# Performance work log

Measured on AMD Instinct MI355X. Metric: run time of the kernel, lower is better.

Reference implementation:

```python
import jax, jax.numpy as jnp
import numpy as np
import math

B, S, D, H = 2, 2048, 1024, 16
HD = D // H  # head_dim = 64


def setup_inputs() -> dict:
    rng = jax.random.key(0)
    ks = jax.random.split(rng, 11)
    std = 1.0 / math.sqrt(D)
    inp = {
        "query": jax.random.normal(ks[0], (B, S, D), dtype=jnp.float32),
        "key": jax.random.normal(ks[1], (B, S, D), dtype=jnp.float32),
        "value": jax.random.normal(ks[2], (B, S, D), dtype=jnp.float32),
        # causal mask: True = masked (ignored), matching masked_fill semantics
        "mask": jnp.triu(jnp.ones((S, S), dtype=bool), k=1),
        "wq": jax.random.normal(ks[3], (D, D), dtype=jnp.float32) * std,
        "bq": jnp.zeros((D,), dtype=jnp.float32),
        "wk": jax.random.normal(ks[4], (D, D), dtype=jnp.float32) * std,
        "bk": jnp.zeros((D,), dtype=jnp.float32),
        "wv": jax.random.normal(ks[5], (D, D), dtype=jnp.float32) * std,
        "bv": jnp.zeros((D,), dtype=jnp.float32),
        "wo": jax.random.normal(ks[6], (D, D), dtype=jnp.float32) * std,
        "bo": jnp.zeros((D,), dtype=jnp.float32),
    }
    return inp


def reference(query, key, value, mask, wq, bq, wk, bk, wv, bv, wo, bo):
    # Linear projections (torch Linear: x @ W.T + b)
    q = jnp.einsum('bsd,ed->bse', query, wq) + bq
    k = jnp.einsum('bsd,ed->bse', key, wk) + bk
    v = jnp.einsum('bsd,ed->bse', value, wv) + bv
    # split heads: (B, S, D) -> (B, H, S, HD)
    q = q.reshape(B, S, H, HD).transpose(0, 2, 1, 3)
    k = k.reshape(B, S, H, HD).transpose(0, 2, 1, 3)
    v = v.reshape(B, S, H, HD).transpose(0, 2, 1, 3)
    # naive attention: materialize full (B, H, Sq, Sk) scores
    scores = jnp.einsum('bhqd,bhkd->bhqk', q, k) / jnp.sqrt(jnp.float32(HD))
    scores = jnp.where(mask[None, None, :, :], -jnp.inf, scores)
    attn = jax.nn.softmax(scores, axis=-1)
    out = jnp.einsum('bhqk,bhkd->bhqd', attn, v)
    out = out.transpose(0, 2, 1, 3).reshape(B, S, D)
    return jnp.einsum('bsd,ed->bse', out, wo) + bo
```

## Files before the change

### kernel.cpp

```cpp
#include <hip/hip_runtime.h>
#include <stdint.h>

#define B_ 2
#define S_ 2048
#define D_ 1024
#define H_ 16
#define HD_ 64
#define M_TOT (B_*S_)

typedef __bf16 bf16;
typedef bf16 bf16x8 __attribute__((ext_vector_type(8)));
typedef float f32x4 __attribute__((ext_vector_type(4)));
typedef float f32x16 __attribute__((ext_vector_type(16)));
typedef unsigned int u32;
typedef unsigned int u32x4v __attribute__((ext_vector_type(4)));

__device__ __forceinline__ void gload_lds16(const void* g, void* l) {
    __builtin_amdgcn_global_load_lds((const __attribute__((address_space(1))) void*)g,
                                     (__attribute__((address_space(3))) void*)l, 16, 0, 0);
}

__device__ __forceinline__ u32 cvtpk_bf16(float lo, float hi) {
    u32 d;
    asm("v_cvt_pk_bf16_f32 %0, %1, %2" : "=v"(d) : "v"(lo), "v"(hi));
    return d;
}

__global__ __launch_bounds__(256) void cvt_kernel(
    const float* __restrict__ q, const float* __restrict__ k, const float* __restrict__ v,
    const float* __restrict__ wq, const float* __restrict__ wk,
    const float* __restrict__ wv, const float* __restrict__ wo,
    bf16* __restrict__ xq, bf16* __restrict__ xk, bf16* __restrict__ xv,
    bf16* __restrict__ wqb, bf16* __restrict__ wkb, bf16* __restrict__ wvb, bf16* __restrict__ wob)
{
    const float* src; bf16* dst; int n;
    switch (blockIdx.y) {
        case 0: src=q;  dst=xq;  n=M_TOT*D_; break;
        case 1: src=k;  dst=xk;  n=M_TOT*D_; break;
        case 2: src=v;  dst=xv;  n=M_TOT*D_; break;
        case 3: src=wq; dst=wqb; n=D_*D_;    break;
        case 4: src=wk; dst=wkb; n=D_*D_;    break;
        case 5: src=wv; dst=wvb; n=D_*D_;    break;
        default: src=wo; dst=wob; n=D_*D_;   break;
    }
    int i = (blockIdx.x*blockDim.x + threadIdx.x)*8;
    if (i >= n) return;
    const f32x4* s4 = (const f32x4*)(src + i);
    f32x4 a = s4[0], b = s4[1];
    bf16x8 o;
    #pragma unroll
    for (int j = 0; j < 4; ++j) { o[j] = (bf16)a[j]; o[j+4] = (bf16)b[j]; }
    *(bf16x8*)(dst + i) = o;
}

__device__ __forceinline__ void gemm_mainloop(const bf16* __restrict__ A, const bf16* __restrict__ Wt,
                                              int brow, int bcol, bf16* As, bf16* Bs,
                                              f32x4 (&acc)[4][4])
{
    const int tid = threadIdx.x;
    const int l = tid & 63, w = tid >> 6;
    const int wr = w >> 1, wc = w & 1;
    const int lr = l & 15, lq = l >> 4;

    for (int k0 = 0; k0 < D_; k0 += 32) {
        #pragma unroll
        for (int i = 0; i < 2; ++i) {
            int id = i*256 + tid;
            int row = id >> 2, c8 = (id & 3) << 3;
            gload_lds16(A  + (size_t)(brow + row)*D_ + k0 + c8, As + id*8);
            gload_lds16(Wt + (size_t)(bcol + row)*D_ + k0 + c8, Bs + id*8);
        }
        __syncthreads();
        bf16x8 af[4], bf[4];
        #pragma unroll
        for (int m = 0; m < 4; ++m)
            af[m] = *(const bf16x8*)&As[(wr*64 + m*16 + lr)*32 + lq*8];
        #pragma unroll
        for (int n = 0; n < 4; ++n)
            bf[n] = *(const bf16x8*)&Bs[(wc*64 + n*16 + lr)*32 + lq*8];
        #pragma unroll
        for (int m = 0; m < 4; ++m)
            #pragma unroll
            for (int n = 0; n < 4; ++n)
                acc[m][n] = __builtin_amdgcn_mfma_f32_16x16x32_bf16(af[m], bf[n], acc[m][n], 0, 0, 0);
        __syncthreads();
    }
}

__global__ __launch_bounds__(256) void gemm_qkv(
    const bf16* __restrict__ xq, const bf16* __restrict__ xk, const bf16* __restrict__ xv,
    const bf16* __restrict__ wqb, const bf16* __restrict__ wkb, const bf16* __restrict__ wvb,
    const float* __restrict__ bq, const float* __restrict__ bk, const float* __restrict__ bv,
    bf16* __restrict__ Qf, bf16* __restrict__ Kf, bf16* __restrict__ Vf)
{
    __shared__ __align__(16) bf16 As[128*32];
    __shared__ __align__(16) bf16 Bs[128*32];
    const int z = blockIdx.z;
    const bf16* A  = (z==0) ? xq  : (z==1) ? xk  : xv;
    const bf16* Wt = (z==0) ? wqb : (z==1) ? wkb : wvb;
    const float* bias = (z==0) ? bq : (z==1) ? bk : bv;

    const int brow = (blockIdx.x & 31)*128;
    const int bcol = (blockIdx.x >> 5)*128;

    f32x4 acc[4][4] = {};
    gemm_mainloop(A, Wt, brow, bcol, As, Bs, acc);

    const int tid = threadIdx.x;
    const int l = tid & 63, w = tid >> 6;
    const int wr = w >> 1, wc = w & 1;
    const int lr = l & 15, lq = l >> 4;

    #pragma unroll
    for (int m = 0; m < 4; ++m)
        #pragma unroll
        for (int n = 0; n < 4; ++n) {
            int col = bcol + wc*64 + n*16 + lr;
            float bv_ = bias[col];
            int h = col >> 6, hd = col & 63;
            #pragma unroll
            for (int r = 0; r < 4; ++r) {
                int row = brow + wr*64 + m*16 + lq*4 + r;
                int b = row >> 11, s = row & 2047;
                float val = acc[m][n][r] + bv_;
                if (z == 0) val *= 0.18033688011112042f;
                size_t hbase = ((size_t)b*H_ + h)*S_*HD_;
                if (z < 2) {
                    int chunk = ((s >> 5) << 2) + (hd >> 4);
                    int lane  = (((hd >> 3) & 1) << 5) | (s & 31);
                    bf16* dst = (z==0) ? Qf : Kf;
                    dst[hbase + (size_t)chunk*512 + lane*8 + (hd & 7)] = (bf16)val;
                } else {
                    int chunk = ((s >> 6) << 3) + (((s >> 4) & 3) << 1) + (hd >> 5);
                    int lane  = (((s >> 3) & 1) << 5) | (hd & 31);
                    Vf[hbase + (size_t)chunk*512 + lane*8 + (s & 7)] = (bf16)val;
                }
            }
        }
}

__global__ __launch_bounds__(256) void gemm_out(
    const bf16* __restrict__ Oat, const bf16* __restrict__ wob,
    const float* __restrict__ bo, float* __restrict__ out)
{
    __shared__ __align__(16) bf16 As[128*32];
    __shared__ __align__(16) bf16 Bs[128*32];
    const int brow = (blockIdx.x & 31)*128;
    const int bcol = (blockIdx.x >> 5)*128;

    f32x4 acc[4][4] = {};
    gemm_mainloop(Oat, wob, brow, bcol, As, Bs, acc);

    const int tid = threadIdx.x;
    const int l = tid & 63, w = tid >> 6;
    const int wr = w >> 1, wc = w & 1;
    const int lr = l & 15, lq = l >> 4;

    #pragma unroll
    for (int m = 0; m < 4; ++m)
        #pragma unroll
        for (int n = 0; n < 4; ++n) {
            int col = bcol + wc*64 + n*16 + lr;
            float bv_ = bo[col];
            #pragma unroll
            for (int r = 0; r < 4; ++r) {
                int row = brow + wr*64 + m*16 + lq*4 + r;
                out[(size_t)row*D_ + col] = acc[m][n][r] + bv_;
            }
        }
}

#define ATTN_BODY(CUR, NXT, KT) do {                                                        \
    const int kc0_ = (KT)*64;                                                               \
    const bool last_ = ((KT) == nkt - 1);                                                   \
    const int ktn_ = ((KT) + 1 < te) ? (KT) + 1 : (KT);                                     \
    bf16x8 va0[4], va1[4];                                                                  \
    _Pragma("unroll")                                                                       \
    for (int c = 0; c < 4; ++c) {                                                           \
        va0[c] = *(const bf16x8*)(Vfp + (size_t)((KT)*8 + c*2 + 0)*512 + l8);               \
        va1[c] = *(const bf16x8*)(Vfp + (size_t)((KT)*8 + c*2 + 1)*512 + l8);               \
    }                                                                                       \
    _Pragma("unroll")                                                                       \
    for (int kv2 = 0; kv2 < 2; ++kv2)                                                       \
        _Pragma("unroll")                                                                   \
        for (int dc = 0; dc < 4; ++dc)                                                      \
            NXT[kv2][dc] = *(const bf16x8*)(Kfp + (size_t)((ktn_*2 + kv2)*4 + dc)*512 + l8);\
    f32x16 ct0 = {}, ct1 = {};                                                              \
    __builtin_amdgcn_s_setprio(1);                                                          \
    _Pragma("unroll")                                                                       \
    for (int dc = 0; dc < 4; ++dc)                                                          \
        ct0 = __builtin_amdgcn_mfma_f32_32x32x16_bf16(CUR[0][dc], qb[dc], ct0, 0, 0, 0);    \
    _Pragma("unroll")                                                                       \
    for (int dc = 0; dc < 4; ++dc)                                                          \
        ct1 = __builtin_amdgcn_mfma_f32_32x32x16_bf16(CUR[1][dc], qb[dc], ct1, 0, 0, 0);    \
    __builtin_amdgcn_s_setprio(0);                                                          \
    if (last_) {                                                                            \
        _Pragma("unroll")                                                                   \
        for (int reg = 0; reg < 16; ++reg) {                                                \
            const int rr = (reg & 3) + 8*(reg >> 2) + 4*hi;                                 \
            if (kc0_ + rr > qrow)      ct0[reg] = -1e30f;                                   \
            if (kc0_ + 32 + rr > qrow) ct1[reg] = -1e30f;                                   \
        }                                                                                   \
    }                                                                                       \
    float t8[8];                                                                            \
    _Pragma("unroll")                                                                       \
    for (int i = 0; i < 8; ++i)                                                             \
        t8[i] = fmaxf(fmaxf(ct0[i], ct0[i+8]), fmaxf(ct1[i], ct1[i+8]));                    \
    float t4a = fmaxf(t8[0], t8[4]), t4b = fmaxf(t8[1], t8[5]);                             \
    float t4c = fmaxf(t8[2], t8[6]), t4d = fmaxf(t8[3], t8[7]);                             \
    float vm = fmaxf(fmaxf(t4a, t4b), fmaxf(t4c, t4d));                                     \
    vm = fmaxf(vm, __shfl_xor(vm, 32));                                                     \
    if (!__all(vm <= mrun + 8.f)) {                                                         \
        float nm = fmaxf(mrun, vm);                                                         \
        float al = exp2f(mrun - nm);                                                        \
        _Pragma("unroll")                                                                   \
        for (int i = 0; i < 16; ++i) { ot0[i] *= al; ot1[i] *= al; }                        \
        lrun *= al;                                                                         \
        mrun = nm;                                                                          \
    }                                                                                       \
    _Pragma("unroll")                                                                       \
    for (int i = 0; i < 16; ++i) {                                                          \
        ct0[i] = exp2f(ct0[i] - mrun);                                                      \
        ct1[i] = exp2f(ct1[i] - mrun);                                                      \
    }                                                                                       \
    float s8[8];                                                                            \
    _Pragma("unroll")                                                                       \
    for (int i = 0; i < 8; ++i)                                                             \
        s8[i] = (ct0[i] + ct0[i+8]) + (ct1[i] + ct1[i+8]);                                  \
    float s4a = s8[0]+s8[4], s4b = s8[1]+s8[5], s4c = s8[2]+s8[6], s4d = s8[3]+s8[7];       \
    float ps = (s4a + s4b) + (s4c + s4d);                                                   \
    ps += __shfl_xor(ps, 32);                                                               \
    lrun += ps;                                                                             \
    u32 own0[8], own1[8], oth0[8], oth1[8];                                                 \
    _Pragma("unroll")                                                                       \
    for (int u = 0; u < 8; ++u) {                                                           \
        own0[u] = cvtpk_bf16(ct0[2*u], ct0[2*u+1]);                                         \
        own1[u] = cvtpk_bf16(ct1[2*u], ct1[2*u+1]);                                         \
    }                                                                                       \
    _Pragma("unroll")                                                                       \
    for (int u = 0; u < 8; ++u) {                                                           \
        oth0[u] = __shfl_xor(own0[u], 32);                                                  \
        oth1[u] = __shfl_xor(own1[u], 32);                                                  \
    }                                                                                       \
    __builtin_amdgcn_s_setprio(1);                                                          \
    _Pragma("unroll")                                                                       \
    for (int c = 0; c < 4; ++c) {                                                           \
        const int b0 = 4*(c & 1);                                                           \
        u32 o0, o1, o2, o3, x0, x1, x2, x3;                                                 \
        if ((c >> 1) == 0) {                                                                \
            o0 = own0[b0]; o1 = own0[b0+1]; o2 = own0[b0+2]; o3 = own0[b0+3];               \
            x0 = oth0[b0]; x1 = oth0[b0+1]; x2 = oth0[b0+2]; x3 = oth0[b0+3];               \
        } else {                                                                            \
            o0 = own1[b0]; o1 = own1[b0+1]; o2 = own1[b0+2]; o3 = own1[b0+3];               \
            x0 = oth1[b0]; x1 = oth1[b0+1]; x2 = oth1[b0+2]; x3 = oth1[b0+3];               \
        }                                                                                   \
        u32 w0 = hi ? x2 : o0;                                                              \
        u32 w1 = hi ? x3 : o1;                                                              \
        u32 w2 = hi ? o2 : x0;                                                              \
        u32 w3 = hi ? o3 : x1;                                                              \
        u32x4v pw = { w0, w1, w2, w3 };                                                     \
        bf16x8 pb = __builtin_bit_cast(bf16x8, pw);                                         \
        ot0 = __builtin_amdgcn_mfma_f32_32x32x16_bf16(va0[c], pb, ot0, 0, 0, 0);            \
        ot1 = __builtin_amdgcn_mfma_f32_32x32x16_bf16(va1[c], pb, ot1, 0, 0, 0);            \
    }                                                                                       \
    __builtin_amdgcn_s_setprio(0);                                                          \
} while (0)

__global__ __launch_bounds__(64, 2) void attn_part(
    const bf16* __restrict__ Qf, const bf16* __restrict__ Kf,
    const bf16* __restrict__ Vf, bf16* __restrict__ Opart, float* __restrict__ Mlf)
{
    const int l = threadIdx.x & 63;
    const int l31 = l & 31, hi = l >> 5;
    const int l8 = l*8;

    const int id = (int)blockIdx.x;
    const int xcd = id & 7;
    const int slot = id >> 3;
    const int bh = xcd + 8*(slot >> 7);
    const int rem = slot & 127;
    const int qt = 63 - (rem >> 1);
    const int half = rem & 1;
    const int q0 = qt*32;
    const int qrow = q0 + l31;
    const int widx = (bh*64 + qt)*2 + half;

    const bf16* Qfp = Qf + (size_t)bh*S_*HD_;
    const bf16* Kfp = Kf + (size_t)bh*S_*HD_;
    const bf16* Vfp = Vf + (size_t)bh*S_*HD_;

    const int nkt = q0/64 + 1;
    const int nh0 = nkt - (nkt >> 1);
    const int ts = half ? nh0 : 0;
    const int te = half ? nkt : nh0;

    bf16x8 qb[4];
    #pragma unroll
    for (int dc = 0; dc < 4; ++dc)
        qb[dc] = *(const bf16x8*)(Qfp + (size_t)(((q0 >> 5) << 2) + dc)*512 + l8);

    f32x16 ot0 = {}, ot1 = {};
    float mrun = -1e30f, lrun = 0.f;

    if (ts < te) {
        bf16x8 ka[2][4], kb[2][4];
        #pragma unroll
        for (int kv2 = 0; kv2 < 2; ++kv2)
            #pragma unroll
            for (int dc = 0; dc < 4; ++dc)
                ka[kv2][dc] = *(const bf16x8*)(Kfp + (size_t)((ts*2 + kv2)*4 + dc)*512 + l8);

        int kt = ts;
        while (kt + 1 < te) {
            ATTN_BODY(ka, kb, kt); ++kt;
            ATTN_BODY(kb, ka, kt); ++kt;
        }
        if (kt < te) {
            ATTN_BODY(ka, kb, kt);
        }
    }

    bf16* Ob = Opart + (size_t)widx*2048;
    #pragma unroll
    for (int rp = 0; rp < 16; ++rp) {
        const int d0 = (rp & 3) + 8*(rp >> 2) + 4*hi;
        Ob[d0*32 + l31]        = (bf16)ot0[rp];
        Ob[(32 + d0)*32 + l31] = (bf16)ot1[rp];
    }
    if (!hi) {
        Mlf[(size_t)widx*64 + l31*2]     = mrun;
        Mlf[(size_t)widx*64 + l31*2 + 1] = lrun;
    }
}

__global__ __launch_bounds__(64) void attn_combine(
    const bf16* __restrict__ Opart, const float* __restrict__ Mlf, bf16* __restrict__ Oat)
{
    const int cb = (int)blockIdx.x;
    const int bh = cb >> 6, qt = cb & 63;
    const int b = bh >> 4, h = bh & 15;
    const int q0 = qt*32;
    const int l = threadIdx.x & 63;
    const int q = l & 31, hi = l >> 5;

    const int w0 = (bh*64 + qt)*2, w1 = w0 + 1;
    const float m0 = Mlf[(size_t)w0*64 + q*2],     l0 = Mlf[(size_t)w0*64 + q*2 + 1];
    const float m1 = Mlf[(size_t)w1*64 + q*2],     l1 = Mlf[(size_t)w1*64 + q*2 + 1];
    const float m = fmaxf(m0, m1);
    const float a0 = exp2f(m0 - m), a1 = exp2f(m1 - m);
    const float inv = 1.f / (l0*a0 + l1*a1);
    const float f0 = a0*inv, f1 = a1*inv;

    const bf16* O0 = Opart + (size_t)w0*2048;
    const bf16* O1 = Opart + (size_t)w1*2048;
    char* rowp = (char*)Oat + (((size_t)(b*S_ + q0 + q)*D_ + h*64 + hi*32)*2);

    #pragma unroll
    for (int i = 0; i < 16; ++i) {
        const int d = hi*32 + 2*i;
        float oA = (float)O0[d*32 + q]*f0       + (float)O1[d*32 + q]*f1;
        float oB = (float)O0[(d+1)*32 + q]*f0   + (float)O1[(d+1)*32 + q]*f1;
        *(u32*)(rowp + 4*i) = cvtpk_bf16(oA, oB);
    }
}

extern "C" void kernel_launch(void* const* d_in, const int* in_sizes, int n_in,
                              void* d_out, int out_size, void* d_ws, size_t ws_size,
                              hipStream_t stream) {
    const float* q  = (const float*)d_in[0];
    const float* k  = (const float*)d_in[1];
    const float* v  = (const float*)d_in[2];
    const float* wq = (const float*)d_in[4];
    const float* bq = (const float*)d_in[5];
    const float* wk = (const float*)d_in[6];
    const float* bk = (const float*)d_in[7];
    const float* wv = (const float*)d_in[8];
    const float* bv = (const float*)d_in[9];
    const float* wo = (const float*)d_in[10];
    const float* bo = (const float*)d_in[11];
    float* out = (float*)d_out;

    char* p = (char*)d_ws;
    const size_t XSZ = (size_t)M_TOT*D_*sizeof(bf16);
    const size_t WSZ = (size_t)D_*D_*sizeof(bf16);
    bf16* xq  = (bf16*)p;
    bf16* xk  = (bf16*)(p + XSZ);
    bf16* xv  = (bf16*)(p + 2*XSZ);
    bf16* wqb = (bf16*)(p + 3*XSZ);
    bf16* wkb = (bf16*)(p + 3*XSZ + WSZ);
    bf16* wvb = (bf16*)(p + 3*XSZ + 2*WSZ);
    bf16* wob = (bf16*)(p + 3*XSZ + 3*WSZ);
    bf16* Qf  = (bf16*)(p + 3*XSZ + 4*WSZ);
    bf16* Kf  = Qf + M_TOT*D_;
    bf16* Vf  = Kf + M_TOT*D_;
    bf16* Oat = Vf + M_TOT*D_;
    bf16*  Opart = (bf16*)p;
    float* Mlf   = (float*)(p + 2*XSZ);

    cvt_kernel<<<dim3(2048, 7), 256, 0, stream>>>(q, k, v, wq, wk, wv, wo,
                                                  xq, xk, xv, wqb, wkb, wvb, wob);
    gemm_qkv<<<dim3(256, 1, 3), 256, 0, stream>>>(xq, xk, xv, wqb, wkb, wvb,
                                                  bq, bk, bv, Qf, Kf, Vf);
    attn_part<<<4096, 64, 0, stream>>>(Qf, Kf, Vf, Opart, Mlf);
    attn_combine<<<2048, 64, 0, stream>>>(Opart, Mlf, Oat);
    gemm_out<<<dim3(256), 256, 0, stream>>>(Oat, wob, bo, out);
}
```

Before: 130.2 us.

## Split attention KV range three ways and double GEMM K-tile depth

The attention partial kernel now splits each query tile's causal KV range into three parts instead of two, launching more single-wave blocks, and the combine kernel merges three partial outputs using their max/sum statistics. Separately, the shared GEMM mainloop loads 64-wide K slices per iteration, which halves the barrier count and doubles the MFMAs issued per sync. This uses more LDS per block and more partial-output traffic. The Mlf buffer is moved so it does not overlap the larger Opart region.

```diff
diff --git a/kernel.cpp b/kernel.cpp
--- a/kernel.cpp
+++ b/kernel.cpp
@@ -7,6 +7,7 @@
 #define H_ 16
 #define HD_ 64
 #define M_TOT (B_*S_)
+#define NSPL 3
 
 typedef __bf16 bf16;
 typedef bf16 bf16x8 __attribute__((ext_vector_type(8)));
@@ -62,27 +63,33 @@
     const int wr = w >> 1, wc = w & 1;
     const int lr = l & 15, lq = l >> 4;
 
-    for (int k0 = 0; k0 < D_; k0 += 32) {
-        #pragma unroll
-        for (int i = 0; i < 2; ++i) {
+    for (int k0 = 0; k0 < D_; k0 += 64) {
+        #pragma unroll
+        for (int i = 0; i < 4; ++i) {
             int id = i*256 + tid;
-            int row = id >> 2, c8 = (id & 3) << 3;
+            int row = id >> 3, c8 = (id & 7) << 3;
             gload_lds16(A  + (size_t)(brow + row)*D_ + k0 + c8, As + id*8);
             gload_lds16(Wt + (size_t)(bcol + row)*D_ + k0 + c8, Bs + id*8);
         }
         __syncthreads();
-        bf16x8 af[4], bf[4];
+        bf16x8 af[4][2], bf[4][2];
         #pragma unroll
         for (int m = 0; m < 4; ++m)
-            af[m] = *(const bf16x8*)&As[(wr*64 + m*16 + lr)*32 + lq*8];
+            #pragma unroll
+            for (int ks = 0; ks < 2; ++ks)
+                af[m][ks] = *(const bf16x8*)&As[(wr*64 + m*16 + lr)*64 + ks*32 + lq*8];
         #pragma unroll
         for (int n = 0; n < 4; ++n)
-            bf[n] = *(const bf16x8*)&Bs[(wc*64 + n*16 + lr)*32 + lq*8];
+            #pragma unroll
+            for (int ks = 0; ks < 2; ++ks)
+                bf[n][ks] = *(const bf16x8*)&Bs[(wc*64 + n*16 + lr)*64 + ks*32 + lq*8];
         #pragma unroll
         for (int m = 0; m < 4; ++m)
             #pragma unroll
             for (int n = 0; n < 4; ++n)
-                acc[m][n] = __builtin_amdgcn_mfma_f32_16x16x32_bf16(af[m], bf[n], acc[m][n], 0, 0, 0);
+                #pragma unroll
+                for (int ks = 0; ks < 2; ++ks)
+                    acc[m][n] = __builtin_amdgcn_mfma_f32_16x16x32_bf16(af[m][ks], bf[n][ks], acc[m][n], 0, 0, 0);
         __syncthreads();
     }
 }
@@ -93,8 +100,8 @@
     const float* __restrict__ bq, const float* __restrict__ bk, const float* __restrict__ bv,
     bf16* __restrict__ Qf, bf16* __restrict__ Kf, bf16* __restrict__ Vf)
 {
-    __shared__ __align__(16) bf16 As[128*32];
-    __shared__ __align__(16) bf16 Bs[128*32];
+    __shared__ __align__(16) bf16 As[128*64];
+    __shared__ __align__(16) bf16 Bs[128*64];
     const int z = blockIdx.z;
     const bf16* A  = (z==0) ? xq  : (z==1) ? xk  : xv;
     const bf16* Wt = (z==0) ? wqb : (z==1) ? wkb : wvb;
@@ -143,8 +150,8 @@
     const bf16* __restrict__ Oat, const bf16* __restrict__ wob,
     const float* __restrict__ bo, float* __restrict__ out)
 {
-    __shared__ __align__(16) bf16 As[128*32];
-    __shared__ __align__(16) bf16 Bs[128*32];
+    __shared__ __align__(16) bf16 As[128*64];
+    __shared__ __align__(16) bf16 Bs[128*64];
     const int brow = (blockIdx.x & 31)*128;
     const int bcol = (blockIdx.x >> 5)*128;
 
@@ -277,22 +284,21 @@
     const int id = (int)blockIdx.x;
     const int xcd = id & 7;
     const int slot = id >> 3;
-    const int bh = xcd + 8*(slot >> 7);
-    const int rem = slot & 127;
-    const int qt = 63 - (rem >> 1);
-    const int half = rem & 1;
+    const int bh = xcd + 8*(slot/192);
+    const int rem = slot % 192;
+    const int qt = 63 - rem/3;
+    const int part = rem % 3;
     const int q0 = qt*32;
     const int qrow = q0 + l31;
-    const int widx = (bh*64 + qt)*2 + half;
+    const int widx = (bh*64 + qt)*NSPL + part;
 
     const bf16* Qfp = Qf + (size_t)bh*S_*HD_;
     const bf16* Kfp = Kf + (size_t)bh*S_*HD_;
     const bf16* Vfp = Vf + (size_t)bh*S_*HD_;
 
     const int nkt = q0/64 + 1;
-    const int nh0 = nkt - (nkt >> 1);
-    const int ts = half ? nh0 : 0;
-    const int te = half ? nkt : nh0;
+    const int ts = (part*nkt)/NSPL;
+    const int te = ((part+1)*nkt)/NSPL;
 
     bf16x8 qb[4];
     #pragma unroll
@@ -343,23 +349,34 @@
     const int l = threadIdx.x & 63;
     const int q = l & 31, hi = l >> 5;
 
-    const int w0 = (bh*64 + qt)*2, w1 = w0 + 1;
-    const float m0 = Mlf[(size_t)w0*64 + q*2],     l0 = Mlf[(size_t)w0*64 + q*2 + 1];
-    const float m1 = Mlf[(size_t)w1*64 + q*2],     l1 = Mlf[(size_t)w1*64 + q*2 + 1];
-    const float m = fmaxf(m0, m1);
-    const float a0 = exp2f(m0 - m), a1 = exp2f(m1 - m);
-    const float inv = 1.f / (l0*a0 + l1*a1);
-    const float f0 = a0*inv, f1 = a1*inv;
-
-    const bf16* O0 = Opart + (size_t)w0*2048;
-    const bf16* O1 = Opart + (size_t)w1*2048;
+    const int wbase = (bh*64 + qt)*NSPL;
+    float mm[NSPL], ll[NSPL];
+    #pragma unroll
+    for (int p = 0; p < NSPL; ++p) {
+        mm[p] = Mlf[(size_t)(wbase+p)*64 + q*2];
+        ll[p] = Mlf[(size_t)(wbase+p)*64 + q*2 + 1];
+    }
+    float m = fmaxf(fmaxf(mm[0], mm[1]), mm[2]);
+    float f[NSPL];
+    float lt = 0.f;
+    #pragma unroll
+    for (int p = 0; p < NSPL; ++p) { f[p] = exp2f(mm[p] - m); lt += ll[p]*f[p]; }
+    const float inv = 1.f / lt;
+    #pragma unroll
+    for (int p = 0; p < NSPL; ++p) f[p] *= inv;
+
     char* rowp = (char*)Oat + (((size_t)(b*S_ + q0 + q)*D_ + h*64 + hi*32)*2);
 
     #pragma unroll
     for (int i = 0; i < 16; ++i) {
         const int d = hi*32 + 2*i;
-        float oA = (float)O0[d*32 + q]*f0       + (float)O1[d*32 + q]*f1;
-        float oB = (float)O0[(d+1)*32 + q]*f0   + (float)O1[(d+1)*32 + q]*f1;
+        float oA = 0.f, oB = 0.f;
+        #pragma unroll
+        for (int p = 0; p < NSPL; ++p) {
+            const bf16* Op = Opart + (size_t)(wbase+p)*2048;
+            oA += (float)Op[d*32 + q]*f[p];
+            oB += (float)Op[(d+1)*32 + q]*f[p];
+        }
         *(u32*)(rowp + 4*i) = cvtpk_bf16(oA, oB);
     }
 }
@@ -395,13 +412,13 @@
     bf16* Vf  = Kf + M_TOT*D_;
     bf16* Oat = Vf + M_TOT*D_;
     bf16*  Opart = (bf16*)p;
-    float* Mlf   = (float*)(p + 2*XSZ);
+    float* Mlf   = (float*)(p + 3*XSZ);
 
     cvt_kernel<<<dim3(2048, 7), 256, 0, stream>>>(q, k, v, wq, wk, wv, wo,
                                                   xq, xk, xv, wqb, wkb, wvb, wob);
     gemm_qkv<<<dim3(256, 1, 3), 256, 0, stream>>>(xq, xk, xv, wqb, wkb, wvb,
                                                   bq, bk, bv, Qf, Kf, Vf);
-    attn_part<<<4096, 64, 0, stream>>>(Qf, Kf, Vf, Opart, Mlf);
+    attn_part<<<32*64*NSPL, 64, 0, stream>>>(Qf, Kf, Vf, Opart, Mlf);
     attn_combine<<<2048, 64, 0, stream>>>(Opart, Mlf, Oat);
     gemm_out<<<dim3(256), 256, 0, stream>>>(Oat, wob, bo, out);
 }
```

Result: slower. 145.4 us (+11.6%).
